# Kernel tuning notes

Measured on AMD Instinct MI355X. Metric: run time of the kernel, lower is better.

Reference implementation:

```python
import jax, jax.numpy as jnp
import numpy as np

B, S = 2, 2048
D_MODEL, N_HEAD = 2048, 16
D_K = D_MODEL // N_HEAD        # 128
D_C, D_CQ = 512, 1024
D_ROPE = 64
D_NOPE = D_K - D_ROPE          # 64
EPS = 1.1920929e-07            # torch.finfo(float32).eps (nn.RMSNorm default)


def rms_norm(x, w):
    var = jnp.mean(x * x, axis=-1, keepdims=True)
    return x * jax.lax.rsqrt(var + EPS) * w


def setup_inputs() -> dict:
    key = jax.random.key(0)
    ks = jax.random.split(key, 16)
    g = lambda k, shape: (jax.random.normal(k, shape, dtype=jnp.float32) * 0.02)
    return {
        "x": jax.random.normal(ks[0], (B, S, D_MODEL), dtype=jnp.float32),
        "q_down_w": g(ks[1], (D_CQ, D_MODEL)),
        "q_down_b": g(ks[2], (D_CQ,)),
        "q_norm_w": jnp.ones((D_CQ,), jnp.float32),
        "q_up_w": g(ks[3], (N_HEAD * D_K, D_CQ)),
        "q_up_b": g(ks[4], (N_HEAD * D_K,)),
        "kv_down_w": g(ks[5], (D_C, D_MODEL)),
        "kv_down_b": g(ks[6], (D_C,)),
        "kv_norm_w": jnp.ones((D_C,), jnp.float32),
        "kv_up_w": g(ks[7], (N_HEAD * (D_NOPE + D_K), D_C)),
        "kv_up_b": g(ks[8], (N_HEAD * (D_NOPE + D_K),)),
        "k_rope_w": g(ks[9], (N_HEAD * D_ROPE, D_MODEL)),
        "k_rope_b": g(ks[10], (N_HEAD * D_ROPE,)),
        "out_w": g(ks[11], (D_MODEL, D_MODEL)),
        "out_b": g(ks[12], (D_MODEL,)),
    }


def reference(x, q_down_w, q_down_b, q_norm_w, q_up_w, q_up_b,
              kv_down_w, kv_down_b, kv_norm_w, kv_up_w, kv_up_b,
              k_rope_w, k_rope_b, out_w, out_b):
    b, s, _ = x.shape
    # Q low-rank path: down -> RMSNorm -> up
    c_q = rms_norm(x @ q_down_w.T + q_down_b, q_norm_w)              # [b,s,d_cq]
    q = (c_q @ q_up_w.T + q_up_b).reshape(b, s, N_HEAD, D_K)
    q = jnp.transpose(q, (0, 2, 1, 3))                               # [b,h,s,d_k]
    q_nope, q_rope = q[..., :D_NOPE], q[..., D_NOPE:]
    # KV low-rank path
    c_kv = rms_norm(x @ kv_down_w.T + kv_down_b, kv_norm_w)          # [b,s,d_c]
    kv = (c_kv @ kv_up_w.T + kv_up_b).reshape(b, s, N_HEAD, D_NOPE + D_K)
    kv = jnp.transpose(kv, (0, 2, 1, 3))                             # [b,h,s,d_nope+d_k]
    k_nope, v = kv[..., :D_NOPE], kv[..., D_NOPE:]
    # decoupled rope subspace (rope=None config: no rotation applied)
    k_rope = (x @ k_rope_w.T + k_rope_b).reshape(b, s, N_HEAD, D_ROPE)
    k_rope = jnp.transpose(k_rope, (0, 2, 1, 3))                     # [b,h,s,d_rope]
    q = jnp.concatenate([q_nope, q_rope], axis=-1)                   # [b,h,s,d_k]
    k = jnp.concatenate([k_nope, k_rope], axis=-1)                   # [b,h,s,d_k]
    # causal attention
    scores = jnp.einsum('bhnd,bhmd->bhnm', q, k) / np.sqrt(D_K).astype(np.float32)
    mask = jnp.tril(jnp.ones((s, s), dtype=bool))
    scores = jnp.where(mask, scores, -jnp.inf)
    probs = jax.nn.softmax(scores, axis=-1)
    attn = jnp.einsum('bhnm,bhmd->bhnd', probs, v)                   # [b,h,s,d_k]
    attn = jnp.transpose(attn, (0, 2, 1, 3)).reshape(b, s, D_MODEL)
    return attn @ out_w.T + out_b
```

## Files before the change

kernel.cpp:

```cpp
#include <hip/hip_runtime.h>
#include <hip/hip_bf16.h>

typedef __attribute__((ext_vector_type(8))) short bf16x8;
typedef __attribute__((ext_vector_type(4))) float f32x4;
typedef __attribute__((ext_vector_type(16))) float f32x16;
typedef unsigned short u16;
typedef unsigned int u32;

#define RMS_EPS 1.1920929e-07f

constexpr int Bb = 2, Ss = 2048, DM = 2048, NH = 16;
constexpr int MROWS = Bb * Ss;

__device__ __forceinline__ u16 f2bf(float f) {
    __hip_bfloat16 h = __float2bfloat16(f);
    return *reinterpret_cast<u16*>(&h);
}

__device__ __forceinline__ float exp2_fast(float x) {
    float r; asm("v_exp_f32 %0, %1" : "=v"(r) : "v"(x)); return r;
}

__device__ __forceinline__ void gload16(const void* g, void* l) {
    __builtin_amdgcn_global_load_lds(
        (const __attribute__((address_space(1))) unsigned int*)g,
        (__attribute__((address_space(3))) unsigned int*)l, 16, 0, 0);
}

__global__ __launch_bounds__(256) void cvt_all(
    const float* __restrict__ s0, u16* __restrict__ d0,
    const float* __restrict__ s1, u16* __restrict__ d1,
    const float* __restrict__ s2, u16* __restrict__ d2,
    const float* __restrict__ s3, u16* __restrict__ d3,
    const float* __restrict__ s4, u16* __restrict__ d4,
    const float* __restrict__ s5, u16* __restrict__ d5,
    const float* __restrict__ s6, u16* __restrict__ d6)
{
    int i = blockIdx.x * 256 + threadIdx.x;
    const float* s; u16* d; int off;
    if (i < 2097152)      { s = s0; d = d0; off = 0; }
    else if (i < 2621440) { s = s1; d = d1; off = 2097152; }
    else if (i < 2883584) { s = s2; d = d2; off = 2621440; }
    else if (i < 3407872) { s = s3; d = d3; off = 2883584; }
    else if (i < 3932160) { s = s4; d = d4; off = 3407872; }
    else if (i < 4325376) { s = s5; d = d5; off = 3932160; }
    else                  { s = s6; d = d6; off = 4325376; }
    int j = i - off;
    float4 v = reinterpret_cast<const float4*>(s)[j];
    ushort4 o;
    o.x = f2bf(v.x); o.y = f2bf(v.y); o.z = f2bf(v.z); o.w = f2bf(v.w);
    reinterpret_cast<ushort4*>(d)[j] = o;
}

__global__ void build_bcat(const float* __restrict__ qb, const float* __restrict__ kvb,
                           const float* __restrict__ krb, float* __restrict__ bcat) {
    int i = blockIdx.x * 256 + threadIdx.x;
    if (i < 1024) bcat[i] = qb[i];
    else if (i < 1536) bcat[i] = kvb[i - 1024];
    else if (i < 2560) bcat[i] = krb[i - 1536];
}

__device__ __forceinline__ void xcd_remap(int& bx, int& by) {
    int nx = gridDim.x, ny = gridDim.y;
    int nwg = nx * ny;
    if ((nwg & 7) != 0) return;
    int flat = blockIdx.x + nx * blockIdx.y;
    int chunk = nwg >> 3;
    int wg = (flat & 7) * chunk + (flat >> 3);
    by = wg % ny;
    bx = wg / ny;
}

template <typename OutT>
__global__ __launch_bounds__(256) void gemm_bt(
    const u16* __restrict__ A, const u16* __restrict__ Bt,
    const float* __restrict__ bias, OutT* __restrict__ C,
    int M, int N, int K)
{
    __shared__ alignas(16) u16 sA[128 * 32];
    __shared__ alignas(16) u16 sB[128 * 32];
    const int tid = threadIdx.x;
    const int lane = tid & 63;
    const int w = tid >> 6;
    const int wr = w >> 1, wc = w & 1;
    const int l16 = lane & 15, lq = lane >> 4;
    int bx = blockIdx.x, by = blockIdx.y;
    xcd_remap(bx, by);
    const int tileM = by * 128;
    const int tileN = bx * 128;

    f32x4 acc[4][4];
#pragma unroll
    for (int m = 0; m < 4; m++)
#pragma unroll
        for (int n = 0; n < 4; n++)
#pragma unroll
            for (int r = 0; r < 4; r++) acc[m][n][r] = 0.f;

    const int srow = w * 16 + (lane >> 2);
    const int scol = (lane & 3) * 8;
    const u16* gA0 = A + (size_t)(tileM + srow) * K + scol;
    const u16* gA1 = A + (size_t)(tileM + srow + 64) * K + scol;
    const u16* gB0 = Bt + (size_t)(tileN + srow) * K + scol;
    const u16* gB1 = Bt + (size_t)(tileN + srow + 64) * K + scol;
    u16* lA0 = sA + w * 512;
    u16* lA1 = sA + 2048 + w * 512;
    u16* lB0 = sB + w * 512;
    u16* lB1 = sB + 2048 + w * 512;

    int aoff[4], boff[4];
#pragma unroll
    for (int m = 0; m < 4; m++) aoff[m] = (wr * 64 + m * 16 + l16) * 32 + lq * 8;
#pragma unroll
    for (int n = 0; n < 4; n++) boff[n] = (wc * 64 + n * 16 + l16) * 32 + lq * 8;

    const int nk = K >> 5;
    for (int kk = 0; kk < nk; ++kk) {
        __syncthreads();
        gload16(gA0, lA0);
        gload16(gA1, lA1);
        gload16(gB0, lB0);
        gload16(gB1, lB1);
        gA0 += 32; gA1 += 32; gB0 += 32; gB1 += 32;
        __syncthreads();
        bf16x8 af[4], bfr[4];
#pragma unroll
        for (int m = 0; m < 4; m++) af[m] = *(const bf16x8*)&sA[aoff[m]];
#pragma unroll
        for (int n = 0; n < 4; n++) bfr[n] = *(const bf16x8*)&sB[boff[n]];
        __builtin_amdgcn_s_setprio(1);
#pragma unroll
        for (int m = 0; m < 4; m++)
#pragma unroll
            for (int n = 0; n < 4; n++)
                acc[m][n] = __builtin_amdgcn_mfma_f32_16x16x32_bf16(af[m], bfr[n], acc[m][n], 0, 0, 0);
        __builtin_amdgcn_s_setprio(0);
    }

#pragma unroll
    for (int n = 0; n < 4; n++) {
        int col = tileN + wc * 64 + n * 16 + l16;
        float bv = bias ? bias[col] : 0.f;
#pragma unroll
        for (int m = 0; m < 4; m++) {
            int rowb = tileM + wr * 64 + m * 16 + (lq << 2);
#pragma unroll
            for (int r = 0; r < 4; r++) {
                float v = acc[m][n][r] + bv;
                if constexpr (sizeof(OutT) == 2)
                    C[(size_t)(rowb + r) * N + col] = (OutT)f2bf(v);
                else
                    C[(size_t)(rowb + r) * N + col] = (OutT)v;
            }
        }
    }
}

__global__ __launch_bounds__(256) void gemm_down(
    const u16* __restrict__ A, const u16* __restrict__ Bt,
    const float* __restrict__ bcat, float* __restrict__ dcat,
    u16* __restrict__ krbuf)
{
    constexpr int K = 2048;
    __shared__ alignas(16) u16 sA[128 * 32];
    __shared__ alignas(16) u16 sB[128 * 32];
    const int tid = threadIdx.x;
    const int lane = tid & 63;
    const int w = tid >> 6;
    const int wr = w >> 1, wc = w & 1;
    const int l16 = lane & 15, lq = lane >> 4;
    int bx = blockIdx.x, by = blockIdx.y;
    xcd_remap(bx, by);
    const int tileM = by * 128;
    const int tileN = bx * 128;

    f32x4 acc[4][4];
#pragma unroll
    for (int m = 0; m < 4; m++)
#pragma unroll
        for (int n = 0; n < 4; n++)
#pragma unroll
            for (int r = 0; r < 4; r++) acc[m][n][r] = 0.f;

    const int srow = w * 16 + (lane >> 2);
    const int scol = (lane & 3) * 8;
    const u16* gA0 = A + (size_t)(tileM + srow) * K + scol;
    const u16* gA1 = A + (size_t)(tileM + srow + 64) * K + scol;
    const u16* gB0 = Bt + (size_t)(tileN + srow) * K + scol;
    const u16* gB1 = Bt + (size_t)(tileN + srow + 64) * K + scol;
    u16* lA0 = sA + w * 512;
    u16* lA1 = sA + 2048 + w * 512;
    u16* lB0 = sB + w * 512;
    u16* lB1 = sB + 2048 + w * 512;

    int aoff[4], boff[4];
#pragma unroll
    for (int m = 0; m < 4; m++) aoff[m] = (wr * 64 + m * 16 + l16) * 32 + lq * 8;
#pragma unroll
    for (int n = 0; n < 4; n++) boff[n] = (wc * 64 + n * 16 + l16) * 32 + lq * 8;

    const int nk = K >> 5;
    for (int kk = 0; kk < nk; ++kk) {
        __syncthreads();
        gload16(gA0, lA0);
        gload16(gA1, lA1);
        gload16(gB0, lB0);
        gload16(gB1, lB1);
        gA0 += 32; gA1 += 32; gB0 += 32; gB1 += 32;
        __syncthreads();
        bf16x8 af[4], bfr[4];
#pragma unroll
        for (int m = 0; m < 4; m++) af[m] = *(const bf16x8*)&sA[aoff[m]];
#pragma unroll
        for (int n = 0; n < 4; n++) bfr[n] = *(const bf16x8*)&sB[boff[n]];
        __builtin_amdgcn_s_setprio(1);
#pragma unroll
        for (int m = 0; m < 4; m++)
#pragma unroll
            for (int n = 0; n < 4; n++)
                acc[m][n] = __builtin_amdgcn_mfma_f32_16x16x32_bf16(af[m], bfr[n], acc[m][n], 0, 0, 0);
        __builtin_amdgcn_s_setprio(0);
    }

    const bool isrope = (tileN >= 1536);
#pragma unroll
    for (int n = 0; n < 4; n++) {
        int col = tileN + wc * 64 + n * 16 + l16;
        float bv = bcat[col];
#pragma unroll
        for (int m = 0; m < 4; m++) {
            int rowb = tileM + wr * 64 + m * 16 + (lq << 2);
#pragma unroll
            for (int r = 0; r < 4; r++) {
                float v = acc[m][n][r] + bv;
                if (!isrope) dcat[(size_t)(rowb + r) * 1536 + col] = v;
                else         krbuf[(size_t)(rowb + r) * 1024 + (col - 1536)] = f2bf(v);
            }
        }
    }
}

template <int C>
__global__ __launch_bounds__(256) void rmsnorm_bf16(
    const float* __restrict__ in, int istride, const float* __restrict__ wgt, u16* __restrict__ out)
{
    const int row = blockIdx.x;
    const int tid = threadIdx.x;
    constexpr int PER = C / 256;
    const float* p = in + (size_t)row * istride;
    float v[PER];
    float ss = 0.f;
#pragma unroll
    for (int i = 0; i < PER; i++) { v[i] = p[tid + i * 256]; ss += v[i] * v[i]; }
#pragma unroll
    for (int o = 32; o; o >>= 1) ss += __shfl_xor(ss, o, 64);
    __shared__ float red[4];
    if ((tid & 63) == 0) red[tid >> 6] = ss;
    __syncthreads();
    float tot = red[0] + red[1] + red[2] + red[3];
    float inv = rsqrtf(tot / (float)C + RMS_EPS);
    u16* q = out + (size_t)row * C;
#pragma unroll
    for (int i = 0; i < PER; i++) {
        int c = tid + i * 256;
        q[c] = f2bf(v[i] * inv * wgt[c]);
    }
}

__global__ __launch_bounds__(256) void transpose_v(
    const u16* __restrict__ kvbuf, u16* __restrict__ vT)
{
    __shared__ alignas(16) u16 tile[64][72];
    const int tid = threadIdx.x;
    const int t0 = blockIdx.x * 64;
    const int h = blockIdx.y >> 1, dh = blockIdx.y & 1;
    const int trow = tid >> 2, c8 = (tid & 3) * 8;
    const u16* src = kvbuf + (size_t)(t0 + trow) * 3072 + h * 192 + 64 + dh * 64 + c8;
    *(bf16x8*)&tile[trow][c8]      = *(const bf16x8*)src;
    *(bf16x8*)&tile[trow][c8 + 32] = *(const bf16x8*)(src + 32);
    __syncthreads();
    const int drow = tid >> 2, tc8 = (tid & 3) * 8;
    bf16x8 a, b2;
#pragma unroll
    for (int j = 0; j < 8; j++) {
        a[j]  = (short)tile[tc8 + j][drow];
        b2[j] = (short)tile[tc8 + 32 + j][drow];
    }
    u16* dst = vT + (size_t)(h * 128 + dh * 64 + drow) * MROWS + t0 + tc8;
    *(bf16x8*)dst = a;
    *(bf16x8*)(dst + 32) = b2;
}

__global__ __launch_bounds__(256, 2) void mla_attn(
    const u16* __restrict__ qbuf,
    const u16* __restrict__ kvbuf,
    const u16* __restrict__ krbuf,
    const u16* __restrict__ vT,
    u16* __restrict__ obuf)
{
    const int bh = blockIdx.x;
    const int y = blockIdx.y;
    const int ii = y & 7, jj = y >> 3;
    const int qt = jj ? (15 - 2 * ii) : (2 * ii);
    const int b = bh >> 4, hh = bh & 15;
    const int tid = threadIdx.x, lane = tid & 63, w = tid >> 6;
    const int l31 = lane & 31, hx = lane >> 5;

    __shared__ alignas(16) u16 sK[64 * 128];
    __shared__ alignas(16) u16 sVt[128 * 64];

    const int rowbase = b * Ss;
    const int q0 = qt * 128;
    const int nkt = 2 * qt + 2;

    const int sr = tid >> 2, sc = (tid & 3) * 32;
    const int vd = tid >> 1, vh = (tid & 1) * 32;
    const float C1 = 0.12751742f;
    const float THRR = 90.5f;

    bf16x8 qf[8];
    {
        const u16* qp = qbuf + (size_t)(rowbase + q0 + w * 32 + l31) * 2048 + hh * 128;
#pragma unroll
        for (int c = 0; c < 8; c++) qf[c] = *(const bf16x8*)(qp + (2 * c + hx) * 8);
    }
    float mi = -3e38f, li = 0.f;
    f32x16 o[4];
#pragma unroll
    for (int d = 0; d < 4; d++)
#pragma unroll
        for (int i = 0; i < 16; i++) o[d][i] = 0.f;

    bf16x8 kr[4], vr[4];
    {
        const int krow = rowbase + sr;
        const u16* src = (sc < 64)
            ? kvbuf + (size_t)krow * 3072 + hh * 192 + sc
            : krbuf + (size_t)krow * 1024 + hh * 64 + (sc - 64);
#pragma unroll
        for (int j = 0; j < 4; j++) kr[j] = *(const bf16x8*)(src + j * 8);
        const u16* vsrc = vT + (size_t)(hh * 128 + vd) * MROWS + rowbase + vh;
#pragma unroll
        for (int j = 0; j < 4; j++) vr[j] = *(const bf16x8*)(vsrc + j * 8);
    }

#pragma unroll 1
    for (int kt = 0; kt < nkt; ++kt) {
        __syncthreads();
#pragma unroll
        for (int j = 0; j < 4; j++) {
            int byteoff = sr * 256 + (sc + j * 8) * 2;
            *(bf16x8*)((char*)sK + (byteoff ^ ((sr & 7) << 4))) = kr[j];
        }
#pragma unroll
        for (int j = 0; j < 4; j++) {
            int byteoff = vd * 128 + (vh + j * 8) * 2;
            *(bf16x8*)((char*)sVt + (byteoff ^ ((vd & 7) << 4))) = vr[j];
        }
        __syncthreads();
        if (kt + 1 < nkt) {
            const int krow = rowbase + (kt + 1) * 64 + sr;
            const u16* src = (sc < 64)
                ? kvbuf + (size_t)krow * 3072 + hh * 192 + sc
                : krbuf + (size_t)krow * 1024 + hh * 64 + (sc - 64);
#pragma unroll
            for (int j = 0; j < 4; j++) kr[j] = *(const bf16x8*)(src + j * 8);
            const u16* vsrc = vT + (size_t)(hh * 128 + vd) * MROWS + rowbase + (kt + 1) * 64 + vh;
#pragma unroll
            for (int j = 0; j < 4; j++) vr[j] = *(const bf16x8*)(vsrc + j * 8);
        }

        const bool alive = (kt * 64) <= (q0 + w * 32 + 31);
        if (alive) {
            f32x16 scf[2];
#pragma unroll
            for (int b2 = 0; b2 < 2; b2++)
#pragma unroll
                for (int i = 0; i < 16; i++) scf[b2][i] = 0.f;
            __builtin_amdgcn_s_setprio(1);
#pragma unroll
            for (int s = 0; s < 8; s++) {
#pragma unroll
                for (int b2 = 0; b2 < 2; b2++) {
                    int krow = b2 * 32 + l31;
                    int kbyte = (krow * 256 + s * 32 + hx * 16) ^ ((l31 & 7) << 4);
                    bf16x8 kf = *(const bf16x8*)((char*)sK + kbyte);
                    scf[b2] = __builtin_amdgcn_mfma_f32_32x32x16_bf16(kf, qf[s], scf[b2], 0, 0, 0);
                }
            }
            __builtin_amdgcn_s_setprio(0);

            if (kt * 64 + 63 > q0 + w * 32) {
                const int qg = q0 + w * 32 + l31;
#pragma unroll
                for (int b2 = 0; b2 < 2; b2++)
#pragma unroll
                    for (int rg = 0; rg < 16; rg++) {
                        int kg = kt * 64 + b2 * 32 + (rg & 3) + 8 * (rg >> 2) + 4 * hx;
                        if (kg > qg) scf[b2][rg] = -3e38f;
                    }
            }
            float mx = mi;
#pragma unroll
            for (int b2 = 0; b2 < 2; b2++)
#pragma unroll
                for (int rg = 0; rg < 16; rg++) mx = fmaxf(mx, scf[b2][rg]);
            mx = fmaxf(mx, __shfl_xor(mx, 32, 64));
            if (!__all(mx - mi <= THRR)) {
                float f = exp2_fast((mi - mx) * C1);
                li *= f;
#pragma unroll
                for (int d = 0; d < 4; d++)
#pragma unroll
                    for (int i = 0; i < 16; i++) o[d][i] *= f;
                mi = mx;
            }
            float mc = mi * C1;
            float rs = 0.f;
#pragma unroll
            for (int b2 = 0; b2 < 2; b2++)
#pragma unroll
                for (int rg = 0; rg < 16; rg++) {
                    float pv = exp2_fast(__fmaf_rn(scf[b2][rg], C1, -mc));
                    scf[b2][rg] = pv;
                    rs += pv;
                }
            rs += __shfl_xor(rs, 32, 64);
            li += rs;

            u32 pk[2][4][2];
#pragma unroll
            for (int b2 = 0; b2 < 2; b2++)
#pragma unroll
                for (int g = 0; g < 4; g++) {
                    pk[b2][g][0] = (u32)f2bf(scf[b2][4 * g + 0]) | ((u32)f2bf(scf[b2][4 * g + 1]) << 16);
                    pk[b2][g][1] = (u32)f2bf(scf[b2][4 * g + 2]) | ((u32)f2bf(scf[b2][4 * g + 3]) << 16);
                }

            __builtin_amdgcn_s_setprio(1);
#pragma unroll
            for (int t = 0; t < 4; t++) {
                const int b2 = t >> 1, s = t & 1;
                u32 send0 = hx ? pk[b2][2 * s][0] : pk[b2][2 * s + 1][0];
                u32 send1 = hx ? pk[b2][2 * s][1] : pk[b2][2 * s + 1][1];
                u32 r0 = (u32)__shfl_xor((int)send0, 32, 64);
                u32 r1 = (u32)__shfl_xor((int)send1, 32, 64);
                union { u32 wd[4]; bf16x8 v; } pu;
                pu.wd[0] = hx ? r0 : pk[b2][2 * s][0];
                pu.wd[1] = hx ? r1 : pk[b2][2 * s][1];
                pu.wd[2] = hx ? pk[b2][2 * s + 1][0] : r0;
                pu.wd[3] = hx ? pk[b2][2 * s + 1][1] : r1;
#pragma unroll
                for (int dblk = 0; dblk < 4; dblk++) {
                    int vrow = dblk * 32 + l31;
                    int vbyte = (vrow * 128 + t * 32 + hx * 16) ^ ((l31 & 7) << 4);
                    bf16x8 vf = *(const bf16x8*)((char*)sVt + vbyte);
                    o[dblk] = __builtin_amdgcn_mfma_f32_32x32x16_bf16(vf, pu.v, o[dblk], 0, 0, 0);
                }
            }
            __builtin_amdgcn_s_setprio(0);
        }
    }
    float invl = 1.f / li;
    u16* op = obuf + (size_t)(rowbase + q0 + w * 32 + l31) * 2048 + hh * 128;
#pragma unroll
    for (int dblk = 0; dblk < 4; dblk++)
#pragma unroll
        for (int rg = 0; rg < 4; rg++) {
            int d0 = dblk * 32 + rg * 8 + hx * 4;
            ushort4 ov;
            ov.x = f2bf(o[dblk][rg * 4 + 0] * invl);
            ov.y = f2bf(o[dblk][rg * 4 + 1] * invl);
            ov.z = f2bf(o[dblk][rg * 4 + 2] * invl);
            ov.w = f2bf(o[dblk][rg * 4 + 3] * invl);
            *(ushort4*)(op + d0) = ov;
        }
}

extern "C" void kernel_launch(void* const* d_in, const int* in_sizes, int n_in,
                              void* d_out, int out_size, void* d_ws, size_t ws_size,
                              hipStream_t stream) {
    const float* x        = (const float*)d_in[0];
    const float* q_down_w = (const float*)d_in[1];
    const float* q_down_b = (const float*)d_in[2];
    const float* q_norm_w = (const float*)d_in[3];
    const float* q_up_w   = (const float*)d_in[4];
    const float* q_up_b   = (const float*)d_in[5];
    const float* kv_down_w= (const float*)d_in[6];
    const float* kv_down_b= (const float*)d_in[7];
    const float* kv_norm_w= (const float*)d_in[8];
    const float* kv_up_w  = (const float*)d_in[9];
    const float* kv_up_b  = (const float*)d_in[10];
    const float* k_rope_w = (const float*)d_in[11];
    const float* k_rope_b = (const float*)d_in[12];
    const float* out_w    = (const float*)d_in[13];
    const float* out_b    = (const float*)d_in[14];

    char* ws = (char*)d_ws;
    u16* xbf    = (u16*)(ws + 0);
    u16* wcat   = (u16*)(ws + 16777216);
    u16* quw    = (u16*)(ws + 27262976);
    u16* kvuw   = (u16*)(ws + 31457280);
    u16* outw   = (u16*)(ws + 34603008);
    float* bcat = (float*)(ws + 42991616);
    float* dcat = (float*)(ws + 43008000);
    u16* cq     = (u16*)(ws + 68173824);
    u16* ckv    = (u16*)(ws + 76562432);
    u16* qbuf   = (u16*)(ws + 80756736);
    u16* kvbuf  = (u16*)(ws + 97533952);
    u16* krbuf  = (u16*)(ws + 122699776);
    u16* vT     = (u16*)(ws + 0);
    u16* attnbuf= (u16*)(ws + 43008000);

    cvt_all<<<20992, 256, 0, stream>>>(
        x, xbf,
        q_down_w,  wcat,
        kv_down_w, wcat + 1024 * 2048,
        k_rope_w,  wcat + 1536 * 2048,
        q_up_w,    quw,
        kv_up_w,   kvuw,
        out_w,     outw);
    build_bcat<<<10, 256, 0, stream>>>(q_down_b, kv_down_b, k_rope_b, bcat);

    gemm_down<<<dim3(20, 32), 256, 0, stream>>>(xbf, wcat, bcat, dcat, krbuf);
    rmsnorm_bf16<1024><<<MROWS, 256, 0, stream>>>(dcat, 1536, q_norm_w, cq);
    rmsnorm_bf16<512><<<MROWS, 256, 0, stream>>>(dcat + 1024, 1536, kv_norm_w, ckv);
    gemm_bt<u16><<<dim3(16, 32), 256, 0, stream>>>(cq, quw, q_up_b, qbuf, MROWS, 2048, 1024);
    gemm_bt<u16><<<dim3(24, 32), 256, 0, stream>>>(ckv, kvuw, kv_up_b, kvbuf, MROWS, 3072, 512);
    transpose_v<<<dim3(64, 32), 256, 0, stream>>>(kvbuf, vT);
    mla_attn<<<dim3(32, 16), 256, 0, stream>>>(qbuf, kvbuf, krbuf, vT, attnbuf);
    gemm_bt<float><<<dim3(16, 32), 256, 0, stream>>>(attnbuf, outw, out_b, (float*)d_out, MROWS, 2048, 2048);
}
```

Measured before the change: 266.8 us.

## Use 128-key tiles with direct global-to-LDS loads in attention kernel

The attention kernel now processes 128 keys per iteration instead of 64 and loads K and V^T tiles straight into shared memory with global_load_lds, replacing the register-staged prefetch. The causal mask is applied only on the diagonal tile, and the per-wave liveness check is dropped. This halves the number of iterations and barriers and removes register staging, at the cost of losing the overlap between next-tile loads and compute, doubling LDS use to 64KB per block, and doing some wasted work on fully masked diagonal sub-blocks.

New measurement: 269.0 us. Within noise of the previous version (+0.9%).

```diff
diff --git a/kernel.cpp b/kernel.cpp
--- a/kernel.cpp
+++ b/kernel.cpp
@@ -306,17 +306,16 @@
     const int tid = threadIdx.x, lane = tid & 63, w = tid >> 6;
     const int l31 = lane & 31, hx = lane >> 5;
 
-    __shared__ alignas(16) u16 sK[64 * 128];
-    __shared__ alignas(16) u16 sVt[128 * 64];
+    __shared__ alignas(16) u16 sK[128 * 128];
+    __shared__ alignas(16) u16 sVt[128 * 128];
 
     const int rowbase = b * Ss;
     const int q0 = qt * 128;
-    const int nkt = 2 * qt + 2;
-
-    const int sr = tid >> 2, sc = (tid & 3) * 32;
-    const int vd = tid >> 1, vh = (tid & 1) * 32;
     const float C1 = 0.12751742f;
     const float THRR = 90.5f;
+
+    const int strow = w * 32 + (lane >> 4);
+    const int stc   = lane & 15;
 
     bf16x8 qf[8];
     {
@@ -331,135 +330,115 @@
 #pragma unroll
         for (int i = 0; i < 16; i++) o[d][i] = 0.f;
 
-    bf16x8 kr[4], vr[4];
-    {
-        const int krow = rowbase + sr;
-        const u16* src = (sc < 64)
-            ? kvbuf + (size_t)krow * 3072 + hh * 192 + sc
-            : krbuf + (size_t)krow * 1024 + hh * 64 + (sc - 64);
-#pragma unroll
-        for (int j = 0; j < 4; j++) kr[j] = *(const bf16x8*)(src + j * 8);
-        const u16* vsrc = vT + (size_t)(hh * 128 + vd) * MROWS + rowbase + vh;
-#pragma unroll
-        for (int j = 0; j < 4; j++) vr[j] = *(const bf16x8*)(vsrc + j * 8);
-    }
-
 #pragma unroll 1
-    for (int kt = 0; kt < nkt; ++kt) {
+    for (int kt = 0; kt <= qt; ++kt) {
         __syncthreads();
 #pragma unroll
-        for (int j = 0; j < 4; j++) {
-            int byteoff = sr * 256 + (sc + j * 8) * 2;
-            *(bf16x8*)((char*)sK + (byteoff ^ ((sr & 7) << 4))) = kr[j];
-        }
-#pragma unroll
-        for (int j = 0; j < 4; j++) {
-            int byteoff = vd * 128 + (vh + j * 8) * 2;
-            *(bf16x8*)((char*)sVt + (byteoff ^ ((vd & 7) << 4))) = vr[j];
+        for (int j = 0; j < 8; j++) {
+            int row = strow + j * 4;
+            int cs = stc ^ (row & 7);
+            int krow = rowbase + kt * 128 + row;
+            const u16* src = (cs < 8)
+                ? kvbuf + (size_t)krow * 3072 + hh * 192 + cs * 8
+                : krbuf + (size_t)krow * 1024 + hh * 64 + (cs - 8) * 8;
+            gload16(src, (char*)sK + w * 8192 + j * 1024);
+        }
+#pragma unroll
+        for (int j = 0; j < 8; j++) {
+            int row = strow + j * 4;
+            int cs = stc ^ (row & 7);
+            const u16* src = vT + (size_t)(hh * 128 + row) * MROWS + rowbase + kt * 128 + cs * 8;
+            gload16(src, (char*)sVt + w * 8192 + j * 1024);
         }
         __syncthreads();
-        if (kt + 1 < nkt) {
-            const int krow = rowbase + (kt + 1) * 64 + sr;
-            const u16* src = (sc < 64)
-                ? kvbuf + (size_t)krow * 3072 + hh * 192 + sc
-                : krbuf + (size_t)krow * 1024 + hh * 64 + (sc - 64);
-#pragma unroll
-            for (int j = 0; j < 4; j++) kr[j] = *(const bf16x8*)(src + j * 8);
-            const u16* vsrc = vT + (size_t)(hh * 128 + vd) * MROWS + rowbase + (kt + 1) * 64 + vh;
-#pragma unroll
-            for (int j = 0; j < 4; j++) vr[j] = *(const bf16x8*)(vsrc + j * 8);
-        }
-
-        const bool alive = (kt * 64) <= (q0 + w * 32 + 31);
-        if (alive) {
-            f32x16 scf[2];
-#pragma unroll
-            for (int b2 = 0; b2 < 2; b2++)
-#pragma unroll
-                for (int i = 0; i < 16; i++) scf[b2][i] = 0.f;
-            __builtin_amdgcn_s_setprio(1);
-#pragma unroll
-            for (int s = 0; s < 8; s++) {
-#pragma unroll
-                for (int b2 = 0; b2 < 2; b2++) {
-                    int krow = b2 * 32 + l31;
-                    int kbyte = (krow * 256 + s * 32 + hx * 16) ^ ((l31 & 7) << 4);
-                    bf16x8 kf = *(const bf16x8*)((char*)sK + kbyte);
-                    scf[b2] = __builtin_amdgcn_mfma_f32_32x32x16_bf16(kf, qf[s], scf[b2], 0, 0, 0);
+
+        f32x16 scf[4];
+#pragma unroll
+        for (int b2 = 0; b2 < 4; b2++)
+#pragma unroll
+            for (int i = 0; i < 16; i++) scf[b2][i] = 0.f;
+        __builtin_amdgcn_s_setprio(1);
+#pragma unroll
+        for (int s = 0; s < 8; s++) {
+#pragma unroll
+            for (int b2 = 0; b2 < 4; b2++) {
+                int krow = b2 * 32 + l31;
+                int kbyte = (krow * 256 + s * 32 + hx * 16) ^ ((l31 & 7) << 4);
+                bf16x8 kf = *(const bf16x8*)((char*)sK + kbyte);
+                scf[b2] = __builtin_amdgcn_mfma_f32_32x32x16_bf16(kf, qf[s], scf[b2], 0, 0, 0);
+            }
+        }
+        __builtin_amdgcn_s_setprio(0);
+
+        if (kt == qt) {
+            const int qg = w * 32 + l31;
+#pragma unroll
+            for (int b2 = 0; b2 < 4; b2++)
+#pragma unroll
+                for (int rg = 0; rg < 16; rg++) {
+                    int kg = b2 * 32 + (rg & 3) + 8 * (rg >> 2) + 4 * hx;
+                    if (kg > qg) scf[b2][rg] = -3e38f;
                 }
+        }
+        float mx = mi;
+#pragma unroll
+        for (int b2 = 0; b2 < 4; b2++)
+#pragma unroll
+            for (int rg = 0; rg < 16; rg++) mx = fmaxf(mx, scf[b2][rg]);
+        mx = fmaxf(mx, __shfl_xor(mx, 32, 64));
+        if (!__all(mx - mi <= THRR)) {
+            float f = exp2_fast((mi - mx) * C1);
+            li *= f;
+#pragma unroll
+            for (int d = 0; d < 4; d++)
+#pragma unroll
+                for (int i = 0; i < 16; i++) o[d][i] *= f;
+            mi = mx;
+        }
+        float mc = mi * C1;
+        float rs = 0.f;
+#pragma unroll
+        for (int b2 = 0; b2 < 4; b2++)
+#pragma unroll
+            for (int rg = 0; rg < 16; rg++) {
+                float pv = exp2_fast(__fmaf_rn(scf[b2][rg], C1, -mc));
+                scf[b2][rg] = pv;
+                rs += pv;
             }
-            __builtin_amdgcn_s_setprio(0);
-
-            if (kt * 64 + 63 > q0 + w * 32) {
-                const int qg = q0 + w * 32 + l31;
-#pragma unroll
-                for (int b2 = 0; b2 < 2; b2++)
-#pragma unroll
-                    for (int rg = 0; rg < 16; rg++) {
-                        int kg = kt * 64 + b2 * 32 + (rg & 3) + 8 * (rg >> 2) + 4 * hx;
-                        if (kg > qg) scf[b2][rg] = -3e38f;
-                    }
+        rs += __shfl_xor(rs, 32, 64);
+        li += rs;
+
+        u32 pk[4][4][2];
+#pragma unroll
+        for (int b2 = 0; b2 < 4; b2++)
+#pragma unroll
+            for (int g = 0; g < 4; g++) {
+                pk[b2][g][0] = (u32)f2bf(scf[b2][4 * g + 0]) | ((u32)f2bf(scf[b2][4 * g + 1]) << 16);
+                pk[b2][g][1] = (u32)f2bf(scf[b2][4 * g + 2]) | ((u32)f2bf(scf[b2][4 * g + 3]) << 16);
             }
-            float mx = mi;
-#pragma unroll
-            for (int b2 = 0; b2 < 2; b2++)
-#pragma unroll
-                for (int rg = 0; rg < 16; rg++) mx = fmaxf(mx, scf[b2][rg]);
-            mx = fmaxf(mx, __shfl_xor(mx, 32, 64));
-            if (!__all(mx - mi <= THRR)) {
-                float f = exp2_fast((mi - mx) * C1);
-                li *= f;
-#pragma unroll
-                for (int d = 0; d < 4; d++)
-#pragma unroll
-                    for (int i = 0; i < 16; i++) o[d][i] *= f;
-                mi = mx;
+
+        __builtin_amdgcn_s_setprio(1);
+#pragma unroll
+        for (int t = 0; t < 8; t++) {
+            const int b2 = t >> 1, s = t & 1;
+            u32 send0 = hx ? pk[b2][2 * s][0] : pk[b2][2 * s + 1][0];
+            u32 send1 = hx ? pk[b2][2 * s][1] : pk[b2][2 * s + 1][1];
+            u32 r0 = (u32)__shfl_xor((int)send0, 32, 64);
+            u32 r1 = (u32)__shfl_xor((int)send1, 32, 64);
+            union { u32 wd[4]; bf16x8 v; } pu;
+            pu.wd[0] = hx ? r0 : pk[b2][2 * s][0];
+            pu.wd[1] = hx ? r1 : pk[b2][2 * s][1];
+            pu.wd[2] = hx ? pk[b2][2 * s + 1][0] : r0;
+            pu.wd[3] = hx ? pk[b2][2 * s + 1][1] : r1;
+#pragma unroll
+            for (int dblk = 0; dblk < 4; dblk++) {
+                int vrow = dblk * 32 + l31;
+                int vbyte = (vrow * 256 + t * 32 + hx * 16) ^ ((l31 & 7) << 4);
+                bf16x8 vf = *(const bf16x8*)((char*)sVt + vbyte);
+                o[dblk] = __builtin_amdgcn_mfma_f32_32x32x16_bf16(vf, pu.v, o[dblk], 0, 0, 0);
             }
-            float mc = mi * C1;
-            float rs = 0.f;
-#pragma unroll
-            for (int b2 = 0; b2 < 2; b2++)
-#pragma unroll
-                for (int rg = 0; rg < 16; rg++) {
-                    float pv = exp2_fast(__fmaf_rn(scf[b2][rg], C1, -mc));
-                    scf[b2][rg] = pv;
-                    rs += pv;
-                }
-            rs += __shfl_xor(rs, 32, 64);
-            li += rs;
-
-            u32 pk[2][4][2];
-#pragma unroll
-            for (int b2 = 0; b2 < 2; b2++)
-#pragma unroll
-                for (int g = 0; g < 4; g++) {
-                    pk[b2][g][0] = (u32)f2bf(scf[b2][4 * g + 0]) | ((u32)f2bf(scf[b2][4 * g + 1]) << 16);
-                    pk[b2][g][1] = (u32)f2bf(scf[b2][4 * g + 2]) | ((u32)f2bf(scf[b2][4 * g + 3]) << 16);
-                }
-
-            __builtin_amdgcn_s_setprio(1);
-#pragma unroll
-            for (int t = 0; t < 4; t++) {
-                const int b2 = t >> 1, s = t & 1;
-                u32 send0 = hx ? pk[b2][2 * s][0] : pk[b2][2 * s + 1][0];
-                u32 send1 = hx ? pk[b2][2 * s][1] : pk[b2][2 * s + 1][1];
-                u32 r0 = (u32)__shfl_xor((int)send0, 32, 64);
-                u32 r1 = (u32)__shfl_xor((int)send1, 32, 64);
-                union { u32 wd[4]; bf16x8 v; } pu;
-                pu.wd[0] = hx ? r0 : pk[b2][2 * s][0];
-                pu.wd[1] = hx ? r1 : pk[b2][2 * s][1];
-                pu.wd[2] = hx ? pk[b2][2 * s + 1][0] : r0;
-                pu.wd[3] = hx ? pk[b2][2 * s + 1][1] : r1;
-#pragma unroll
-                for (int dblk = 0; dblk < 4; dblk++) {
-                    int vrow = dblk * 32 + l31;
-                    int vbyte = (vrow * 128 + t * 32 + hx * 16) ^ ((l31 & 7) << 4);
-                    bf16x8 vf = *(const bf16x8*)((char*)sVt + vbyte);
-                    o[dblk] = __builtin_amdgcn_mfma_f32_32x32x16_bf16(vf, pu.v, o[dblk], 0, 0, 0);
-                }
-            }
-            __builtin_amdgcn_s_setprio(0);
-        }
+        }
+        __builtin_amdgcn_s_setprio(0);
     }
     float invl = 1.f / li;
     u16* op = obuf + (size_t)(rowbase + q0 + w * 32 + l31) * 2048 + hh * 128;
```

## Double-buffer LDS tiles in GEMM kernels to overlap loads with MFMA

Applied to the files above, without the earlier changes.

Both the generic GEMM and the fused down-projection GEMM now use two LDS buffers per operand. The next K-slice is prefetched with global_load_lds while MFMAs run on the current slice, and the per-iteration barrier count drops from two to one. This aims to hide global-memory latency behind compute, at the cost of doubled LDS usage per block, which may reduce occupancy. Whether the async load completes before the post-compute barrier depends on the compiler inserting vmcnt waits.

After: 262.3 us (median of 2 runs). Within noise of the previous version (-1.7%).

```diff
diff --git a/kernel.cpp b/kernel.cpp
--- a/kernel.cpp
+++ b/kernel.cpp
@@ -77,8 +77,8 @@
     const float* __restrict__ bias, OutT* __restrict__ C,
     int M, int N, int K)
 {
-    __shared__ alignas(16) u16 sA[128 * 32];
-    __shared__ alignas(16) u16 sB[128 * 32];
+    __shared__ alignas(16) u16 sA[2][128 * 32];
+    __shared__ alignas(16) u16 sB[2][128 * 32];
     const int tid = threadIdx.x;
     const int lane = tid & 63;
     const int w = tid >> 6;
@@ -103,10 +103,10 @@
     const u16* gA1 = A + (size_t)(tileM + srow + 64) * K + scol;
     const u16* gB0 = Bt + (size_t)(tileN + srow) * K + scol;
     const u16* gB1 = Bt + (size_t)(tileN + srow + 64) * K + scol;
-    u16* lA0 = sA + w * 512;
-    u16* lA1 = sA + 2048 + w * 512;
-    u16* lB0 = sB + w * 512;
-    u16* lB1 = sB + 2048 + w * 512;
+    u16* lA0 = &sA[0][0] + w * 512;
+    u16* lA1 = &sA[0][0] + 2048 + w * 512;
+    u16* lB0 = &sB[0][0] + w * 512;
+    u16* lB1 = &sB[0][0] + 2048 + w * 512;
 
     int aoff[4], boff[4];
 #pragma unroll
@@ -115,19 +115,31 @@
     for (int n = 0; n < 4; n++) boff[n] = (wc * 64 + n * 16 + l16) * 32 + lq * 8;
 
     const int nk = K >> 5;
+    gload16(gA0, lA0);
+    gload16(gA1, lA1);
+    gload16(gB0, lB0);
+    gload16(gB1, lB1);
+    __syncthreads();
+    int cur = 0;
     for (int kk = 0; kk < nk; ++kk) {
-        __syncthreads();
-        gload16(gA0, lA0);
-        gload16(gA1, lA1);
-        gload16(gB0, lB0);
-        gload16(gB1, lB1);
-        gA0 += 32; gA1 += 32; gB0 += 32; gB1 += 32;
-        __syncthreads();
+        if (kk + 1 < nk) {
+            int nb = (cur ^ 1) * 4096;
+            const u16* a0 = gA0 + (size_t)(kk + 1) * 32;
+            const u16* a1 = gA1 + (size_t)(kk + 1) * 32;
+            const u16* b0 = gB0 + (size_t)(kk + 1) * 32;
+            const u16* b1 = gB1 + (size_t)(kk + 1) * 32;
+            gload16(a0, lA0 + nb);
+            gload16(a1, lA1 + nb);
+            gload16(b0, lB0 + nb);
+            gload16(b1, lB1 + nb);
+        }
+        const u16* bA = &sA[0][0] + cur * 4096;
+        const u16* bB = &sB[0][0] + cur * 4096;
         bf16x8 af[4], bfr[4];
 #pragma unroll
-        for (int m = 0; m < 4; m++) af[m] = *(const bf16x8*)&sA[aoff[m]];
-#pragma unroll
-        for (int n = 0; n < 4; n++) bfr[n] = *(const bf16x8*)&sB[boff[n]];
+        for (int m = 0; m < 4; m++) af[m] = *(const bf16x8*)&bA[aoff[m]];
+#pragma unroll
+        for (int n = 0; n < 4; n++) bfr[n] = *(const bf16x8*)&bB[boff[n]];
         __builtin_amdgcn_s_setprio(1);
 #pragma unroll
         for (int m = 0; m < 4; m++)
@@ -135,6 +147,8 @@
             for (int n = 0; n < 4; n++)
                 acc[m][n] = __builtin_amdgcn_mfma_f32_16x16x32_bf16(af[m], bfr[n], acc[m][n], 0, 0, 0);
         __builtin_amdgcn_s_setprio(0);
+        __syncthreads();
+        cur ^= 1;
     }
 
 #pragma unroll
@@ -162,8 +176,8 @@
     u16* __restrict__ krbuf)
 {
     constexpr int K = 2048;
-    __shared__ alignas(16) u16 sA[128 * 32];
-    __shared__ alignas(16) u16 sB[128 * 32];
+    __shared__ alignas(16) u16 sA[2][128 * 32];
+    __shared__ alignas(16) u16 sB[2][128 * 32];
     const int tid = threadIdx.x;
     const int lane = tid & 63;
     const int w = tid >> 6;
@@ -188,10 +202,10 @@
     const u16* gA1 = A + (size_t)(tileM + srow + 64) * K + scol;
     const u16* gB0 = Bt + (size_t)(tileN + srow) * K + scol;
     const u16* gB1 = Bt + (size_t)(tileN + srow + 64) * K + scol;
-    u16* lA0 = sA + w * 512;
-    u16* lA1 = sA + 2048 + w * 512;
-    u16* lB0 = sB + w * 512;
-    u16* lB1 = sB + 2048 + w * 512;
+    u16* lA0 = &sA[0][0] + w * 512;
+    u16* lA1 = &sA[0][0] + 2048 + w * 512;
+    u16* lB0 = &sB[0][0] + w * 512;
+    u16* lB1 = &sB[0][0] + 2048 + w * 512;
 
     int aoff[4], boff[4];
 #pragma unroll
@@ -200,19 +214,31 @@
     for (int n = 0; n < 4; n++) boff[n] = (wc * 64 + n * 16 + l16) * 32 + lq * 8;
 
     const int nk = K >> 5;
+    gload16(gA0, lA0);
+    gload16(gA1, lA1);
+    gload16(gB0, lB0);
+    gload16(gB1, lB1);
+    __syncthreads();
+    int cur = 0;
     for (int kk = 0; kk < nk; ++kk) {
-        __syncthreads();
-        gload16(gA0, lA0);
-        gload16(gA1, lA1);
-        gload16(gB0, lB0);
-        gload16(gB1, lB1);
-        gA0 += 32; gA1 += 32; gB0 += 32; gB1 += 32;
-        __syncthreads();
+        if (kk + 1 < nk) {
+            int nb = (cur ^ 1) * 4096;
+            const u16* a0 = gA0 + (size_t)(kk + 1) * 32;
+            const u16* a1 = gA1 + (size_t)(kk + 1) * 32;
+            const u16* b0 = gB0 + (size_t)(kk + 1) * 32;
+            const u16* b1 = gB1 + (size_t)(kk + 1) * 32;
+            gload16(a0, lA0 + nb);
+            gload16(a1, lA1 + nb);
+            gload16(b0, lB0 + nb);
+            gload16(b1, lB1 + nb);
+        }
+        const u16* bA = &sA[0][0] + cur * 4096;
+        const u16* bB = &sB[0][0] + cur * 4096;
         bf16x8 af[4], bfr[4];
 #pragma unroll
-        for (int m = 0; m < 4; m++) af[m] = *(const bf16x8*)&sA[aoff[m]];
-#pragma unroll
-        for (int n = 0; n < 4; n++) bfr[n] = *(const bf16x8*)&sB[boff[n]];
+        for (int m = 0; m < 4; m++) af[m] = *(const bf16x8*)&bA[aoff[m]];
+#pragma unroll
+        for (int n = 0; n < 4; n++) bfr[n] = *(const bf16x8*)&bB[boff[n]];
         __builtin_amdgcn_s_setprio(1);
 #pragma unroll
         for (int m = 0; m < 4; m++)
@@ -220,6 +246,8 @@
             for (int n = 0; n < 4; n++)
                 acc[m][n] = __builtin_amdgcn_mfma_f32_16x16x32_bf16(af[m], bfr[n], acc[m][n], 0, 0, 0);
         __builtin_amdgcn_s_setprio(0);
+        __syncthreads();
+        cur ^= 1;
     }
 
     const bool isrope = (tileN >= 1536);
```
